# Optimization experiments

Measured on AMD Instinct MI355X. Metric: run time of the kernel, lower is better.

The kernel has to match this reference:

```python
import jax, jax.numpy as jnp
import numpy as np
import math

D = 1024   # input dim
R = 256    # latent dim
K = 8192   # codebook size
N = 32768  # batch of vectors
BETA = 0.25


def setup_inputs() -> dict:
    key = jax.random.key(0)
    kx, kw, kc = jax.random.split(key, 3)
    x = jax.random.normal(kx, (N, D), dtype=jnp.float32)
    W = jax.random.normal(kw, (R, D), dtype=jnp.float32) / math.sqrt(D)
    code = jax.random.normal(kc, (K, R), dtype=jnp.float32) * 0.1
    return {"x": x, "W": W, "code": code}


def reference(x, W, code):
    # encode: z = x @ W^T  -> [N, R]
    z = jnp.einsum('nd,rd->nr', x, W)
    # pairwise squared distances to codebook: [N, K]
    d2 = (jnp.sum(z * z, axis=1, keepdims=True)
          + jnp.sum(code * code, axis=1)[None, :]
          - 2.0 * jnp.einsum('nr,kr->nk', z, code))
    idx = jnp.argmin(d2, axis=1)          # [N] int
    q = code[idx]                          # [N, R] gather
    # straight-through estimator
    zhat = z + jax.lax.stop_gradient(q - z)
    # decode: x_hat = zhat @ W  -> [N, D]
    x_hat = jnp.einsum('nr,rd->nd', zhat, W)
    rec = jnp.mean((x_hat - x) ** 2)
    codebook_loss = jnp.mean((q - jax.lax.stop_gradient(z)) ** 2)
    commit = jnp.mean((z - jax.lax.stop_gradient(q)) ** 2)
    loss = rec + codebook_loss + BETA * commit
    return (loss, rec, z, q, idx)
```

## Files before the change

### kernel.cpp

```cpp
#include <hip/hip_runtime.h>

#define NN 32768
#define DD 1024
#define RR 256
#define KK 8192

typedef float f32x4 __attribute__((ext_vector_type(4)));
typedef _Float16 half8 __attribute__((ext_vector_type(8)));
typedef _Float16 half4_t __attribute__((ext_vector_type(4)));

#define OFF_Z   2L
#define OFF_Q   (2L + (long)NN * RR)
#define OFF_IDX (2L + 2L * (long)NN * RR)

#define O_WT   0L
#define O_CF   524288L
#define O_CN   4718592L
#define O_A    4751360L
#define O_B    4882432L
#define O_M1   4915200L
#define O_KEY  5046272L
#define O_CNT  5308416L
#define O_LIST 5308432L
#define LIST_CAP 262144

#define TAU_S 0.025f

__global__ void k_wt(const float* __restrict__ W, _Float16* __restrict__ Wt) {
  __shared__ float tile[64][65];
  int d0 = blockIdx.x * 64, r0 = blockIdx.y * 64;
  int t = threadIdx.x;
#pragma unroll
  for (int it = 0; it < 16; ++it) {
    int i = t + it * 256;
    int r = i >> 6, d = i & 63;
    tile[r][d] = W[(long)(r0 + r) * DD + d0 + d];
  }
  __syncthreads();
#pragma unroll
  for (int it = 0; it < 16; ++it) {
    int i = t + it * 256;
    int d = i >> 6, r = i & 63;
    Wt[(long)(d0 + d) * RR + r0 + r] = (_Float16)tile[r][d];
  }
}

__global__ void k_code(const float* __restrict__ code, _Float16* __restrict__ cfs,
                       float* __restrict__ cnorm) {
  int k = blockIdx.x;
  int l = threadIdx.x;
  f32x4 v = ((const f32x4*)code)[(long)k * 64 + l];
  half4_t h;
#pragma unroll
  for (int j = 0; j < 4; ++j) h[j] = (_Float16)v[j];
  long dst = ((long)(k >> 4) << 12) + ((long)(l >> 3) << 9) +
             (((l >> 1) & 3) << 7) + ((k & 15) << 3) + ((l & 1) << 2);
  *(half4_t*)(cfs + dst) = h;
  float s = v[0]*v[0] + v[1]*v[1] + v[2]*v[2] + v[3]*v[3];
#pragma unroll
  for (int off = 1; off < 64; off <<= 1) s += __shfl_xor(s, off);
  if (l == 0) cnorm[k] = s;
}

__global__ __launch_bounds__(256, 3)
void k_npz(const float* __restrict__ x, const float* __restrict__ W,
           float* __restrict__ z) {
#pragma clang fp contract(off)
  __shared__ float wsl[128][65];
  __shared__ float xsl[32][64];
  int nb = blockIdx.x * 32;
  int rh = blockIdx.y * 128;
  int t = threadIdx.x;
  int rp = t & 63;
  int nh = t >> 6;
  f32x4 acc[8][2];
#pragma unroll
  for (int n = 0; n < 8; ++n)
#pragma unroll
    for (int q = 0; q < 2; ++q) acc[n][q] = (f32x4){0.f, 0.f, 0.f, 0.f};

  for (int ch = 0; ch < 16; ++ch) {
    __syncthreads();
#pragma unroll
    for (int it = 0; it < 8; ++it) {
      int idx = t + it * 256;
      int r = idx >> 4, kk = (idx & 15) << 2;
      *(f32x4*)&wsl[r][kk] = *(const f32x4*)(W + (long)(rh + r) * DD + ch * 64 + kk);
    }
#pragma unroll
    for (int it = 0; it < 2; ++it) {
      int idx = t + it * 256;
      int r = idx >> 4, kk = (idx & 15) << 2;
      *(f32x4*)&xsl[r][kk] = *(const f32x4*)(x + (long)(nb + r) * DD + ch * 64 + kk);
    }
    __syncthreads();
#pragma unroll 4
    for (int g = 0; g < 16; ++g) {
      f32x4 w0 = *(const f32x4*)&wsl[rp][g * 4];
      f32x4 w1 = *(const f32x4*)&wsl[rp + 64][g * 4];
#pragma unroll
      for (int n = 0; n < 8; ++n) {
        f32x4 xv = *(const f32x4*)&xsl[nh * 8 + n][g * 4];
        f32x4 p0 = xv * w0;
        acc[n][0] = acc[n][0] + p0;
        f32x4 p1 = xv * w1;
        acc[n][1] = acc[n][1] + p1;
      }
    }
  }
#pragma unroll
  for (int n = 0; n < 8; ++n)
#pragma unroll
    for (int q = 0; q < 2; ++q) {
      float sa = acc[n][q][0] + acc[n][q][1];
      float sb = acc[n][q][2] + acc[n][q][3];
      z[(long)(nb + nh * 8 + n) * RR + rh + rp + q * 64] = sa + sb;
    }
}

__device__ __forceinline__ float np_pw256_sq(const float* __restrict__ p) {
#pragma clang fp contract(off)
  float blk[2];
#pragma unroll
  for (int h = 0; h < 2; ++h) {
    const float* q = p + h * 128;
    float r[8];
#pragma unroll
    for (int j = 0; j < 8; ++j) { float v = q[j]; r[j] = v * v; }
    for (int i = 8; i < 128; i += 8) {
#pragma unroll
      for (int j = 0; j < 8; ++j) { float v = q[i + j]; r[j] = r[j] + v * v; }
    }
    float ta = r[0] + r[1], tb = r[2] + r[3], tc = r[4] + r[5], td = r[6] + r[7];
    blk[h] = (ta + tb) + (tc + td);
  }
  return blk[0] + blk[1];
}

__global__ void k_sumA(const float* __restrict__ z, float* __restrict__ A) {
  int n = blockIdx.x * 256 + threadIdx.x;
  A[n] = np_pw256_sq(z + (long)n * RR);
}

__global__ void k_sumB(const float* __restrict__ code, float* __restrict__ B) {
  int k = blockIdx.x * 256 + threadIdx.x;
  B[k] = np_pw256_sq(code + (long)k * RR);
}

__global__ __launch_bounds__(256, 2)
void k_minval(const float* __restrict__ z, const _Float16* __restrict__ cfs,
              const float* __restrict__ cnorm, float* __restrict__ m1arr) {
  __shared__ float sm1[4][64];
  int n0 = blockIdx.x * 64;
  int tid = threadIdx.x;
  int l = tid & 63, w = tid >> 6;
  int lr = l & 15, lg = l >> 4;

  half8 za[4][8];
#pragma unroll
  for (int rf = 0; rf < 4; ++rf) {
    const float* p = z + (long)(n0 + rf * 16 + lr) * RR + lg * 8;
#pragma unroll
    for (int ks = 0; ks < 8; ++ks) {
      f32x4 v0 = *(const f32x4*)(p + ks * 32);
      f32x4 v1 = *(const f32x4*)(p + ks * 32 + 4);
#pragma unroll
      for (int j = 0; j < 4; ++j) {
        za[rf][ks][j]     = (_Float16)v0[j];
        za[rf][ks][4 + j] = (_Float16)v1[j];
      }
    }
  }

  float m1[16];
#pragma unroll
  for (int s = 0; s < 16; ++s) m1[s] = 3.4e38f;
  f32x4 zero = {0.f, 0.f, 0.f, 0.f};

  for (int ct = 0; ct < 128; ++ct) {
    int col0 = ct * 64 + w * 16;
    int c16 = ct * 4 + w;
    const _Float16* bp = cfs + ((long)c16 << 12) + (l << 3);
    float cn = cnorm[col0 + lr];
    f32x4 a[4];
#pragma unroll
    for (int rf = 0; rf < 4; ++rf) a[rf] = zero;
#pragma unroll
    for (int ks = 0; ks < 8; ++ks) {
      half8 b = *(const half8*)(bp + ((long)ks << 9));
#pragma unroll
      for (int rf = 0; rf < 4; ++rf)
        a[rf] = __builtin_amdgcn_mfma_f32_16x16x32_f16(za[rf][ks], b, a[rf], 0, 0, 0);
    }
#pragma unroll
    for (int rf = 0; rf < 4; ++rf)
#pragma unroll
      for (int j = 0; j < 4; ++j) {
        float s = fmaf(-2.f, a[rf][j], cn);
        m1[rf * 4 + j] = fminf(m1[rf * 4 + j], s);
      }
  }

#pragma unroll
  for (int sl = 0; sl < 16; ++sl) {
    float a1 = m1[sl];
#pragma unroll
    for (int off = 1; off < 16; off <<= 1) a1 = fminf(a1, __shfl_xor(a1, off));
    if (lr == 0) sm1[w][(sl >> 2) * 16 + lg * 4 + (sl & 3)] = a1;
  }
  __syncthreads();
  if (tid < 64)
    m1arr[n0 + tid] = fminf(fminf(sm1[0][tid], sm1[1][tid]),
                            fminf(sm1[2][tid], sm1[3][tid]));
}

__global__ __launch_bounds__(256, 2)
void k_collect(const float* __restrict__ z, const _Float16* __restrict__ cfs,
               const float* __restrict__ cnorm, const float* __restrict__ m1arr,
               int* __restrict__ listcnt, unsigned* __restrict__ list, int cap) {
  int n0 = blockIdx.x * 64;
  int tid = threadIdx.x;
  int l = tid & 63, w = tid >> 6;
  int lr = l & 15, lg = l >> 4;

  half8 za[4][8];
#pragma unroll
  for (int rf = 0; rf < 4; ++rf) {
    const float* p = z + (long)(n0 + rf * 16 + lr) * RR + lg * 8;
#pragma unroll
    for (int ks = 0; ks < 8; ++ks) {
      f32x4 v0 = *(const f32x4*)(p + ks * 32);
      f32x4 v1 = *(const f32x4*)(p + ks * 32 + 4);
#pragma unroll
      for (int j = 0; j < 4; ++j) {
        za[rf][ks][j]     = (_Float16)v0[j];
        za[rf][ks][4 + j] = (_Float16)v1[j];
      }
    }
  }

  int rows[16];
  float thr[16];
#pragma unroll
  for (int sl = 0; sl < 16; ++sl) {
    rows[sl] = n0 + (sl >> 2) * 16 + lg * 4 + (sl & 3);
    thr[sl] = m1arr[rows[sl]] + TAU_S;
  }
  f32x4 zero = {0.f, 0.f, 0.f, 0.f};

  for (int ct = 0; ct < 128; ++ct) {
    int col0 = ct * 64 + w * 16;
    int c16 = ct * 4 + w;
    const _Float16* bp = cfs + ((long)c16 << 12) + (l << 3);
    float cn = cnorm[col0 + lr];
    int cand = col0 + lr;
    f32x4 a[4];
#pragma unroll
    for (int rf = 0; rf < 4; ++rf) a[rf] = zero;
#pragma unroll
    for (int ks = 0; ks < 8; ++ks) {
      half8 b = *(const half8*)(bp + ((long)ks << 9));
#pragma unroll
      for (int rf = 0; rf < 4; ++rf)
        a[rf] = __builtin_amdgcn_mfma_f32_16x16x32_f16(za[rf][ks], b, a[rf], 0, 0, 0);
    }
#pragma unroll
    for (int rf = 0; rf < 4; ++rf)
#pragma unroll
      for (int j = 0; j < 4; ++j) {
        int sl = rf * 4 + j;
        float s = fmaf(-2.f, a[rf][j], cn);
        if (s < thr[sl]) {
          int pos = atomicAdd(listcnt, 1);
          if (pos < cap) list[pos] = ((unsigned)rows[sl] << 13) | (unsigned)cand;
        }
      }
  }
}

__global__ void k_npd2(const float* __restrict__ z, const float* __restrict__ code,
                       const float* __restrict__ A, const float* __restrict__ B,
                       const int* __restrict__ listcnt, const unsigned* __restrict__ list,
                       unsigned long long* __restrict__ keys, int cap) {
#pragma clang fp contract(off)
  int n = *listcnt; if (n > cap) n = cap;
  for (int i = blockIdx.x * 256 + threadIdx.x; i < n; i += gridDim.x * 256) {
    unsigned e = list[i];
    int row = (int)(e >> 13), k = (int)(e & 8191u);
    const float* zp = z + (long)row * RR;
    const float* cp = code + (long)k * RR;
    float s0 = 0.f, s1 = 0.f, s2 = 0.f, s3 = 0.f;
    for (int g = 0; g < 64; ++g) {
      f32x4 zv = *(const f32x4*)(zp + g * 4);
      f32x4 cv = *(const f32x4*)(cp + g * 4);
      s0 = s0 + zv[0] * cv[0];
      s1 = s1 + zv[1] * cv[1];
      s2 = s2 + zv[2] * cv[2];
      s3 = s3 + zv[3] * cv[3];
    }
    float C = (s0 + s1) + (s2 + s3);
    float t1 = A[row] + B[k];
    float d2 = t1 - 2.0f * C;
    unsigned long long key = ((unsigned long long)__float_as_uint(d2) << 13) |
                             (unsigned long long)(unsigned)k;
    atomicMin(&keys[row], key);
  }
}

__global__ void k_write(const unsigned long long* __restrict__ keys,
                        float* __restrict__ idxf) {
  int n = blockIdx.x * 256 + threadIdx.x;
  idxf[n] = (float)(unsigned)(keys[n] & 8191ULL);
}

__global__ void k_gather(const float* __restrict__ code, const float* __restrict__ z,
                         const float* __restrict__ idxf, float* __restrict__ q,
                         float* __restrict__ cbsum) {
  int t = threadIdx.x;
  int rid = blockIdx.x * 4 + (t >> 6);
  int l = t & 63;
  int k = (int)idxf[rid];
  f32x4 cv = ((const f32x4*)code)[(long)k * 64 + l];
  f32x4 zv = ((const f32x4*)z)[(long)rid * 64 + l];
  ((f32x4*)q)[(long)rid * 64 + l] = cv;
  f32x4 d = cv - zv;
  float s = d[0]*d[0] + d[1]*d[1] + d[2]*d[2] + d[3]*d[3];
#pragma unroll
  for (int off = 1; off < 64; off <<= 1) s += __shfl_xor(s, off);
  __shared__ float sw[4];
  if (l == 0) sw[t >> 6] = s;
  __syncthreads();
  if (t == 0) atomicAdd(cbsum, sw[0] + sw[1] + sw[2] + sw[3]);
}

__global__ __launch_bounds__(512, 2)
void k_rec(const float* __restrict__ q, const _Float16* __restrict__ Wt,
           const float* __restrict__ x, float* __restrict__ recsum) {
  int n0 = blockIdx.x * 128;
  int d0 = blockIdx.y * 512;
  int tid = threadIdx.x;
  int l = tid & 63, w = tid >> 6;
  int wr = w >> 2, wc = w & 3;
  int lr = l & 15, lg = l >> 4;
  f32x4 zero = {0.f, 0.f, 0.f, 0.f};
  f32x4 acc[4][8];
#pragma unroll
  for (int a = 0; a < 4; ++a)
#pragma unroll
    for (int b = 0; b < 8; ++b) acc[a][b] = zero;

  for (int kk = 0; kk < 8; ++kk) {
    half8 aq[4];
#pragma unroll
    for (int rf = 0; rf < 4; ++rf) {
      const float* p = q + (long)(n0 + wr * 64 + rf * 16 + lr) * RR + kk * 32 + lg * 8;
      f32x4 v0 = *(const f32x4*)p;
      f32x4 v1 = *(const f32x4*)(p + 4);
#pragma unroll
      for (int j = 0; j < 4; ++j) {
        aq[rf][j]     = (_Float16)v0[j];
        aq[rf][4 + j] = (_Float16)v1[j];
      }
    }
#pragma unroll
    for (int cfg = 0; cfg < 8; ++cfg) {
      const _Float16* bp = Wt + (long)(d0 + wc * 128 + cfg * 16 + lr) * RR + kk * 32 + lg * 8;
      half8 b = *(const half8*)bp;
#pragma unroll
      for (int rf = 0; rf < 4; ++rf)
        acc[rf][cfg] = __builtin_amdgcn_mfma_f32_16x16x32_f16(aq[rf], b, acc[rf][cfg], 0, 0, 0);
    }
  }
  float s = 0.f;
#pragma unroll
  for (int rf = 0; rf < 4; ++rf)
#pragma unroll
    for (int cfg = 0; cfg < 8; ++cfg)
#pragma unroll
      for (int j = 0; j < 4; ++j) {
        int n = n0 + wr * 64 + rf * 16 + lg * 4 + j;
        int d = d0 + wc * 128 + cfg * 16 + lr;
        float df = acc[rf][cfg][j] - x[(long)n * DD + d];
        s = fmaf(df, df, s);
      }
#pragma unroll
  for (int off = 1; off < 64; off <<= 1) s += __shfl_xor(s, off);
  __shared__ float sw[8];
  if (l == 0) sw[w] = s;
  __syncthreads();
  if (tid == 0) {
    float t8 = 0.f;
#pragma unroll
    for (int i = 0; i < 8; ++i) t8 += sw[i];
    atomicAdd(recsum, t8);
  }
}

__global__ void k_final(const float* __restrict__ rs, const float* __restrict__ cbs,
                        float* __restrict__ out) {
  if (threadIdx.x == 0 && blockIdx.x == 0) {
    float rec = *rs * (1.0f / 33554432.0f);
    float cb  = *cbs * (1.0f / 8388608.0f);
    out[0] = rec + 1.25f * cb;
    out[1] = rec;
  }
}

extern "C" void kernel_launch(void* const* d_in, const int* in_sizes, int n_in,
                              void* d_out, int out_size, void* d_ws, size_t ws_size,
                              hipStream_t stream) {
  (void)in_sizes; (void)n_in; (void)out_size; (void)ws_size;
  const float* x    = (const float*)d_in[0];
  const float* W    = (const float*)d_in[1];
  const float* code = (const float*)d_in[2];
  float* out = (float*)d_out;
  char* ws = (char*)d_ws;

  _Float16* Wt = (_Float16*)(ws + O_WT);
  _Float16* cfs = (_Float16*)(ws + O_CF);
  float* cnorm = (float*)(ws + O_CN);
  float* A = (float*)(ws + O_A);
  float* B = (float*)(ws + O_B);
  float* m1arr = (float*)(ws + O_M1);
  unsigned long long* keys = (unsigned long long*)(ws + O_KEY);
  int* listcnt = (int*)(ws + O_CNT);
  float* recsum = (float*)(ws + O_CNT + 4);
  float* cbsum  = (float*)(ws + O_CNT + 8);
  unsigned* list = (unsigned*)(ws + O_LIST);

  float* zp = out + OFF_Z;
  float* qp = out + OFF_Q;
  float* ip = out + OFF_IDX;

  hipMemsetAsync(ws + O_CNT, 0, 16, stream);
  hipMemsetAsync(ws + O_KEY, 0xFF, (size_t)NN * 8, stream);

  k_wt<<<dim3(16, 4), dim3(256), 0, stream>>>(W, Wt);
  k_code<<<dim3(KK), dim3(64), 0, stream>>>(code, cfs, cnorm);
  k_npz<<<dim3(1024, 2), dim3(256), 0, stream>>>(x, W, zp);
  k_sumA<<<dim3(128), dim3(256), 0, stream>>>(zp, A);
  k_sumB<<<dim3(32), dim3(256), 0, stream>>>(code, B);
  k_minval<<<dim3(512), dim3(256), 0, stream>>>(zp, cfs, cnorm, m1arr);
  k_collect<<<dim3(512), dim3(256), 0, stream>>>(zp, cfs, cnorm, m1arr, listcnt, list, LIST_CAP);
  k_npd2<<<dim3(1024), dim3(256), 0, stream>>>(zp, code, A, B, listcnt, list, keys, LIST_CAP);
  k_write<<<dim3(128), dim3(256), 0, stream>>>(keys, ip);
  k_gather<<<dim3(8192), dim3(256), 0, stream>>>(code, zp, ip, qp, cbsum);
  k_rec<<<dim3(256, 2), dim3(512), 0, stream>>>(qp, Wt, x, recsum);
  k_final<<<dim3(1), dim3(64), 0, stream>>>(recsum, cbsum, out);
}
```

Measured before the change: 1.205 ms.

## Track top-two distances in first pass and recheck only ambiguous rows

The first fp16 MFMA distance pass now tracks the best and second-best score plus the argmin index per row. Rows whose top-two gap is at least the tolerance get their index written directly. Only rows with a small gap are flagged, and only those go through the second full-codebook collect pass and the exact fp32 recheck. This drops most of the second 32768x8192 MFMA pass. Capping flagged rows at FCAP risks wrong indices if more rows are ambiguous than the cap allows.

```diff
diff --git a/kernel.cpp b/kernel.cpp
--- a/kernel.cpp
+++ b/kernel.cpp
@@ -21,8 +21,10 @@
 #define O_M1   4915200L
 #define O_KEY  5046272L
 #define O_CNT  5308416L
-#define O_LIST 5308432L
+#define O_FLAG 5308432L
+#define O_LIST 5373952L
 #define LIST_CAP 262144
+#define FCAP 16384
 
 #define TAU_S 0.025f
 
@@ -148,9 +150,11 @@
 }
 
 __global__ __launch_bounds__(256, 2)
-void k_minval(const float* __restrict__ z, const _Float16* __restrict__ cfs,
-              const float* __restrict__ cnorm, float* __restrict__ m1arr) {
-  __shared__ float sm1[4][64];
+void k_argmin(const float* __restrict__ z, const _Float16* __restrict__ cfs,
+              const float* __restrict__ cnorm, float* __restrict__ m1arr,
+              float* __restrict__ idxf, int* __restrict__ flagcnt,
+              int* __restrict__ flags, int fcap) {
+  __shared__ float sm1[4][64], sm2[4][64], si1[4][64];
   int n0 = blockIdx.x * 64;
   int tid = threadIdx.x;
   int l = tid & 63, w = tid >> 6;
@@ -172,9 +176,9 @@
     }
   }
 
-  float m1[16];
-#pragma unroll
-  for (int s = 0; s < 16; ++s) m1[s] = 3.4e38f;
+  float m1[16], m2[16], i1[16];
+#pragma unroll
+  for (int s = 0; s < 16; ++s) { m1[s] = 3.4e38f; m2[s] = 3.4e38f; i1[s] = 0.f; }
   f32x4 zero = {0.f, 0.f, 0.f, 0.f};
 
   for (int ct = 0; ct < 128; ++ct) {
@@ -182,6 +186,7 @@
     int c16 = ct * 4 + w;
     const _Float16* bp = cfs + ((long)c16 << 12) + (l << 3);
     float cn = cnorm[col0 + lr];
+    float fi = (float)(col0 + lr);
     f32x4 a[4];
 #pragma unroll
     for (int rf = 0; rf < 4; ++rf) a[rf] = zero;
@@ -196,29 +201,66 @@
     for (int rf = 0; rf < 4; ++rf)
 #pragma unroll
       for (int j = 0; j < 4; ++j) {
+        int sl = rf * 4 + j;
         float s = fmaf(-2.f, a[rf][j], cn);
-        m1[rf * 4 + j] = fminf(m1[rf * 4 + j], s);
+        float om1 = m1[sl];
+        m2[sl] = fminf(m2[sl], fmaxf(s, om1));
+        bool lt = s < om1;
+        m1[sl] = lt ? s : om1;
+        i1[sl] = lt ? fi : i1[sl];
       }
   }
 
 #pragma unroll
   for (int sl = 0; sl < 16; ++sl) {
-    float a1 = m1[sl];
-#pragma unroll
-    for (int off = 1; off < 16; off <<= 1) a1 = fminf(a1, __shfl_xor(a1, off));
-    if (lr == 0) sm1[w][(sl >> 2) * 16 + lg * 4 + (sl & 3)] = a1;
+    float a1 = m1[sl], a2 = m2[sl], ai = i1[sl];
+#pragma unroll
+    for (int off = 1; off < 16; off <<= 1) {
+      float b1 = __shfl_xor(a1, off);
+      float b2 = __shfl_xor(a2, off);
+      float bi = __shfl_xor(ai, off);
+      float nm2 = fminf(fminf(a2, b2), fmaxf(a1, b1));
+      bool take = (b1 < a1) || ((b1 == a1) && (bi < ai));
+      a1 = take ? b1 : a1;
+      ai = take ? bi : ai;
+      a2 = nm2;
+    }
+    if (lr == 0) {
+      int lrow = (sl >> 2) * 16 + lg * 4 + (sl & 3);
+      sm1[w][lrow] = a1; sm2[w][lrow] = a2; si1[w][lrow] = ai;
+    }
   }
   __syncthreads();
-  if (tid < 64)
-    m1arr[n0 + tid] = fminf(fminf(sm1[0][tid], sm1[1][tid]),
-                            fminf(sm1[2][tid], sm1[3][tid]));
+  if (tid < 64) {
+    float a1 = sm1[0][tid], a2 = sm2[0][tid], ai = si1[0][tid];
+#pragma unroll
+    for (int ww = 1; ww < 4; ++ww) {
+      float b1 = sm1[ww][tid], b2 = sm2[ww][tid], bi = si1[ww][tid];
+      float nm2 = fminf(fminf(a2, b2), fmaxf(a1, b1));
+      bool take = (b1 < a1) || ((b1 == a1) && (bi < ai));
+      a1 = take ? b1 : a1;
+      ai = take ? bi : ai;
+      a2 = nm2;
+    }
+    int row = n0 + tid;
+    idxf[row] = ai;
+    m1arr[row] = a1;
+    if (a2 - a1 < TAU_S) {
+      int p = atomicAdd(flagcnt, 1);
+      if (p < fcap) flags[p] = row;
+    }
+  }
 }
 
 __global__ __launch_bounds__(256, 2)
 void k_collect(const float* __restrict__ z, const _Float16* __restrict__ cfs,
                const float* __restrict__ cnorm, const float* __restrict__ m1arr,
-               int* __restrict__ listcnt, unsigned* __restrict__ list, int cap) {
+               const int* __restrict__ flagcnt, const int* __restrict__ flags,
+               int fcap, int* __restrict__ listcnt, unsigned* __restrict__ list,
+               int cap) {
+  int n = *flagcnt; if (n > fcap) n = fcap;
   int n0 = blockIdx.x * 64;
+  if (n0 >= n) return;
   int tid = threadIdx.x;
   int l = tid & 63, w = tid >> 6;
   int lr = l & 15, lg = l >> 4;
@@ -226,7 +268,9 @@
   half8 za[4][8];
 #pragma unroll
   for (int rf = 0; rf < 4; ++rf) {
-    const float* p = z + (long)(n0 + rf * 16 + lr) * RR + lg * 8;
+    int fidx = n0 + rf * 16 + lr;
+    int zrow = (fidx < n) ? flags[fidx] : 0;
+    const float* p = z + (long)zrow * RR + lg * 8;
 #pragma unroll
     for (int ks = 0; ks < 8; ++ks) {
       f32x4 v0 = *(const f32x4*)(p + ks * 32);
@@ -239,12 +283,14 @@
     }
   }
 
-  int rows[16];
+  unsigned rows[16];
   float thr[16];
 #pragma unroll
   for (int sl = 0; sl < 16; ++sl) {
-    rows[sl] = n0 + (sl >> 2) * 16 + lg * 4 + (sl & 3);
-    thr[sl] = m1arr[rows[sl]] + TAU_S;
+    int fidx = n0 + (sl >> 2) * 16 + lg * 4 + (sl & 3);
+    bool v = fidx < n;
+    rows[sl] = v ? (unsigned)flags[fidx] : 0u;
+    thr[sl] = v ? m1arr[rows[sl]] + TAU_S : -3.4e38f;
   }
   f32x4 zero = {0.f, 0.f, 0.f, 0.f};
 
@@ -253,7 +299,7 @@
     int c16 = ct * 4 + w;
     const _Float16* bp = cfs + ((long)c16 << 12) + (l << 3);
     float cn = cnorm[col0 + lr];
-    int cand = col0 + lr;
+    unsigned cand = (unsigned)(col0 + lr);
     f32x4 a[4];
 #pragma unroll
     for (int rf = 0; rf < 4; ++rf) a[rf] = zero;
@@ -272,7 +318,7 @@
         float s = fmaf(-2.f, a[rf][j], cn);
         if (s < thr[sl]) {
           int pos = atomicAdd(listcnt, 1);
-          if (pos < cap) list[pos] = ((unsigned)rows[sl] << 13) | (unsigned)cand;
+          if (pos < cap) list[pos] = (rows[sl] << 13) | cand;
         }
       }
   }
@@ -307,10 +353,15 @@
   }
 }
 
-__global__ void k_write(const unsigned long long* __restrict__ keys,
-                        float* __restrict__ idxf) {
-  int n = blockIdx.x * 256 + threadIdx.x;
-  idxf[n] = (float)(unsigned)(keys[n] & 8191ULL);
+__global__ void k_fix(const int* __restrict__ flagcnt, const int* __restrict__ flags,
+                      const unsigned long long* __restrict__ keys,
+                      float* __restrict__ idxf, int fcap) {
+  int n = *flagcnt; if (n > fcap) n = fcap;
+  for (int i = blockIdx.x * 256 + threadIdx.x; i < n; i += gridDim.x * 256) {
+    int row = flags[i];
+    unsigned long long k = keys[row];
+    if (k != ~0ULL) idxf[row] = (float)(unsigned)(k & 8191ULL);
+  }
 }
 
 __global__ void k_gather(const float* __restrict__ code, const float* __restrict__ z,
@@ -424,8 +475,10 @@
   float* m1arr = (float*)(ws + O_M1);
   unsigned long long* keys = (unsigned long long*)(ws + O_KEY);
   int* listcnt = (int*)(ws + O_CNT);
-  float* recsum = (float*)(ws + O_CNT + 4);
-  float* cbsum  = (float*)(ws + O_CNT + 8);
+  int* flagcnt = (int*)(ws + O_CNT + 4);
+  float* recsum = (float*)(ws + O_CNT + 8);
+  float* cbsum  = (float*)(ws + O_CNT + 12);
+  int* flags = (int*)(ws + O_FLAG);
   unsigned* list = (unsigned*)(ws + O_LIST);
 
   float* zp = out + OFF_Z;
@@ -440,10 +493,10 @@
   k_npz<<<dim3(1024, 2), dim3(256), 0, stream>>>(x, W, zp);
   k_sumA<<<dim3(128), dim3(256), 0, stream>>>(zp, A);
   k_sumB<<<dim3(32), dim3(256), 0, stream>>>(code, B);
-  k_minval<<<dim3(512), dim3(256), 0, stream>>>(zp, cfs, cnorm, m1arr);
-  k_collect<<<dim3(512), dim3(256), 0, stream>>>(zp, cfs, cnorm, m1arr, listcnt, list, LIST_CAP);
-  k_npd2<<<dim3(1024), dim3(256), 0, stream>>>(zp, code, A, B, listcnt, list, keys, LIST_CAP);
-  k_write<<<dim3(128), dim3(256), 0, stream>>>(keys, ip);
+  k_argmin<<<dim3(512), dim3(256), 0, stream>>>(zp, cfs, cnorm, m1arr, ip, flagcnt, flags, FCAP);
+  k_collect<<<dim3(FCAP / 64), dim3(256), 0, stream>>>(zp, cfs, cnorm, m1arr, flagcnt, flags, FCAP, listcnt, list, LIST_CAP);
+  k_npd2<<<dim3(256), dim3(256), 0, stream>>>(zp, code, A, B, listcnt, list, keys, LIST_CAP);
+  k_fix<<<dim3(64), dim3(256), 0, stream>>>(flagcnt, flags, keys, ip, FCAP);
   k_gather<<<dim3(8192), dim3(256), 0, stream>>>(code, zp, ip, qp, cbsum);
   k_rec<<<dim3(256, 2), dim3(512), 0, stream>>>(qp, Wt, x, recsum);
   k_final<<<dim3(1), dim3(64), 0, stream>>>(recsum, cbsum, out);
```

Result: faster. 1.009 ms (-16.2%).
